# Kernel tuning notes

Hardware: AMD Instinct MI355X
Metric: run time of the kernel (lower is better)

Reference implementation:

```python
import jax, jax.numpy as jnp
import numpy as np

N_NODES = 50000
N_EDGES = 800000
FEAT_SIZE = 4096
EMB = 30          # embedding_size
HID = 80          # hidden_size
VOCAB = 10
HEADS = 2
TEMP = 1.0
GAT_SLOPE = 0.2   # DGL GATConv leaky_relu negative_slope
CONV_SLOPE = 0.01 # torch LeakyReLU default


def _lrelu(x, s):
    return jnp.where(x >= 0, x, s * x)


def gat_layer(feat, W, al, ar, b, src, dst, n_nodes):
    """DGL GATConv: feat [N, ..., Fin] -> [N, ..., H, Fout].
    W: [Fin, H*Fout]; al, ar, b: [H, Fout]."""
    H, F = al.shape
    z = jnp.tensordot(feat, W, axes=1).reshape(feat.shape[:-1] + (H, F))  # [N,...,H,F]
    el = (z * al).sum(-1, keepdims=True)  # [N,...,H,1]
    er = (z * ar).sum(-1, keepdims=True)
    e = _lrelu(el[src] + er[dst], GAT_SLOPE)            # [E,...,H,1]
    emax = jax.ops.segment_max(e, dst, num_segments=n_nodes)
    ex = jnp.exp(e - emax[dst])
    denom = jax.ops.segment_sum(ex, dst, num_segments=n_nodes)
    alpha = ex / denom[dst]                              # edge softmax per dst
    rst = jax.ops.segment_sum(z[src] * alpha, dst, num_segments=n_nodes)
    return rst + b


def setup_inputs() -> dict:
    key = jax.random.key(0)
    ks = jax.random.split(key, 24)
    s = 0.1
    return {
        "x": jax.random.normal(ks[0], (2, FEAT_SIZE), jnp.float32),
        "vocab": jax.random.normal(ks[1], (VOCAB,), jnp.float32),
        "node_feats": jax.random.normal(ks[2], (2, N_NODES, 3), jnp.float32),
        "src": jax.random.randint(ks[3], (2, N_EDGES), 0, N_NODES, jnp.int32),
        "dst": jax.random.randint(ks[4], (2, N_EDGES), 0, N_NODES, jnp.int32),
        "W_lin1": jax.random.normal(ks[5], (FEAT_SIZE, EMB), jnp.float32) * s,
        "Wc1": jax.random.normal(ks[6], (HID, 2), jnp.float32) * s,
        "Wc2": jax.random.normal(ks[7], (HID,), jnp.float32) * s,
        "gat1_W": jax.random.normal(ks[8], (3, HEADS * HID), jnp.float32) * s,
        "gat1_al": jax.random.normal(ks[9], (HEADS, HID), jnp.float32) * s,
        "gat1_ar": jax.random.normal(ks[10], (HEADS, HID), jnp.float32) * s,
        "gat1_b": jax.random.normal(ks[11], (HEADS, HID), jnp.float32) * s,
        "gat2_W": jax.random.normal(ks[12], (HID, HEADS * EMB), jnp.float32) * s,
        "gat2_al": jax.random.normal(ks[13], (HEADS, EMB), jnp.float32) * s,
        "gat2_ar": jax.random.normal(ks[14], (HEADS, EMB), jnp.float32) * s,
        "gat2_b": jax.random.normal(ks[15], (HEADS, EMB), jnp.float32) * s,
        "Wg1": jax.random.normal(ks[16], (2 * EMB, EMB), jnp.float32) * s,
        "bg1": jax.random.normal(ks[17], (EMB,), jnp.float32) * s,
        "W2": jax.random.normal(ks[18], (2 * EMB + VOCAB, HID), jnp.float32) * s,
        "W3": jax.random.normal(ks[19], (HID, 2), jnp.float32) * s,
    }


def reference(x, vocab, node_feats, src, dst, W_lin1, Wc1, Wc2,
              gat1_W, gat1_al, gat1_ar, gat1_b,
              gat2_W, gat2_al, gat2_ar, gat2_b,
              Wg1, bg1, W2, W3):
    # deterministic order = [0, 1] (original shuffles); order.index(0) == 0
    # image branch: per-game embedding -> [2, EMB]
    emb = x @ W_lin1                          # [2, EMB]
    h = _lrelu(Wc1 @ emb, CONV_SLOPE)         # im_conv1: [HID, EMB]
    h = _lrelu(Wc2 @ h, CONV_SLOPE)           # im_conv2: [EMB]
    # graph branch: two GAT layers per graph, mean over nodes, take head 0
    gr_emb = []
    for i in range(2):
        g1 = gat_layer(node_feats[i], gat1_W, gat1_al, gat1_ar, gat1_b,
                       src[i], dst[i], N_NODES)          # [N, H, HID]
        g1 = jax.nn.relu(g1)
        g2 = gat_layer(g1, gat2_W, gat2_al, gat2_ar, gat2_b,
                       src[i], dst[i], N_NODES)          # [N, H, H, EMB]
        a = g2.mean(axis=0)[0, 0]                        # mean_nodes then a[0][0][0] -> [EMB]
        gr_emb.append(a)
    gr = jnp.concatenate(gr_emb) @ Wg1 + bg1             # [EMB]
    hc = jnp.concatenate([gr, h, vocab])                 # [2*EMB + VOCAB]
    logits = jax.nn.log_softmax(((hc @ W2) @ W3) * (1.0 / TEMP), axis=0)
    return logits, 0
```

## Files before the change

kernel.cpp:

```cpp
#include <hip/hip_runtime.h>
#include <math.h>

#define NN 50000
#define NE 800000

#define CH 196
#define C  256
#define CAP 3600
#define BSL 8192

__device__ __forceinline__ float lrelu(float x, float s) { return x >= 0.f ? x : s * x; }

__global__ __launch_bounds__(1024) void k_pre(
        const float* __restrict__ x, const float* __restrict__ Wl,
        const float* __restrict__ nodef,
        const float* __restrict__ W1, const float* __restrict__ al1,
        const float* __restrict__ ar1,
        const int* __restrict__ src, const int* __restrict__ dst,
        float* __restrict__ imgp, float* __restrict__ feat4,
        float* __restrict__ er1, unsigned* __restrict__ gctr,
        unsigned* __restrict__ dbin, unsigned* __restrict__ sbin) {
    int bid = blockIdx.x, t = threadIdx.x;
    if (bid < 16) {
        __shared__ float part[32][64];
        int kk = t & 31, rq = t >> 5;
        int r0 = bid * 256;
        float a0 = 0.f, a1 = 0.f;
        if (kk < 30) {
            for (int i = 0; i < 8; ++i) {
                int r = r0 + rq * 8 + i;
                float wv = Wl[r * 30 + kk];
                a0 += x[r] * wv;
                a1 += x[4096 + r] * wv;
            }
        }
        part[rq][kk] = a0;
        part[rq][32 + kk] = a1;
        __syncthreads();
        if (t < 60) {
            int g = t / 30, k = t - g * 30;
            float s = 0.f;
            #pragma unroll
            for (int rr = 0; rr < 32; ++rr) s += part[rr][g * 32 + k];
            imgp[bid * 64 + g * 32 + k] = s;
        }
    } else if (bid < 114) {
        __shared__ float sP[6];
        if (t < 6) {
            int c = t >> 1;
            const float* av = (t & 1) ? ar1 : al1;
            float s = 0.f;
            for (int f = 0; f < 80; ++f) s += W1[c * 160 + f] * av[f];
            sP[(t & 1) * 3 + c] = s;
        }
        __syncthreads();
        int flat = (bid - 16) * 1024 + t;
        if (flat < 2 * NN) {
            int g = flat / NN;
            int n = flat - g * NN;
            const float* f = nodef + (size_t)flat * 3;
            float f0 = f[0], f1 = f[1], f2 = f[2];
            *(float4*)(feat4 + (size_t)flat * 4) =
                make_float4(f0, f1, f2, f0 * sP[0] + f1 * sP[1] + f2 * sP[2]);
            er1[g * NN + n] = f0 * sP[3] + f1 * sP[4] + f2 * sP[5];
        }
    } else {
        __shared__ unsigned scnt[C];
        __shared__ unsigned sstart[C + 1];
        __shared__ unsigned sbase[C];
        __shared__ unsigned sofs[C];
        __shared__ unsigned ssort[BSL];
        int b3 = bid - 114;
        int a = b3 / 196;
        int rem = b3 - a * 196;
        int g = rem / 98;
        int bx = rem - g * 98;
        if (t < C) scnt[t] = 0;
        __syncthreads();
        const int* ip = (a ? src : dst) + (size_t)g * NE;
        const int* pp = (a ? dst : src) + (size_t)g * NE;
        unsigned* bin = (a ? sbin : dbin);
        int cbase = (a * 2 + g) * C;
        int bbase = g * C;
        int e0 = bx * BSL + t * 8;
        int nv = 0;
        if (e0 < NE) nv = (NE - e0) < 8 ? (NE - e0) : 8;
        unsigned pk[8];
        if (nv == 8) {
            int4 v0 = *(const int4*)(ip + e0), v1 = *(const int4*)(ip + e0 + 4);
            int4 q0 = *(const int4*)(pp + e0), q1 = *(const int4*)(pp + e0 + 4);
            int dj[8] = {v0.x, v0.y, v0.z, v0.w, v1.x, v1.y, v1.z, v1.w};
            int pj[8] = {q0.x, q0.y, q0.z, q0.w, q1.x, q1.y, q1.z, q1.w};
            #pragma unroll
            for (int j = 0; j < 8; ++j) {
                unsigned c = (unsigned)dj[j] / CH;
                pk[j] = (c << 24) | (((unsigned)dj[j] - c * CH) << 16) | (unsigned)pj[j];
                atomicAdd(&scnt[c], 1u);
            }
        } else {
            for (int j = 0; j < nv; ++j) {
                int dv = ip[e0 + j], pv = pp[e0 + j];
                unsigned c = (unsigned)dv / CH;
                pk[j] = (c << 24) | (((unsigned)dv - c * CH) << 16) | (unsigned)pv;
                atomicAdd(&scnt[c], 1u);
            }
        }
        __syncthreads();
        if (t == 0) {
            unsigned run = 0;
            for (int j = 0; j < C; ++j) { sstart[j] = run; run += scnt[j]; }
            sstart[C] = run;
        }
        __syncthreads();
        if (t < C) {
            sbase[t] = atomicAdd(&gctr[cbase + t], scnt[t]);
            sofs[t] = sstart[t];
        }
        __syncthreads();
        for (int j = 0; j < nv; ++j) {
            unsigned c = pk[j] >> 24;
            unsigned slot = atomicAdd(&sofs[c], 1u);
            ssort[slot] = pk[j];
        }
        __syncthreads();
        unsigned total = sstart[C];
        for (unsigned i = t; i < total; i += 1024) {
            unsigned v = ssort[i];
            unsigned c = v >> 24;
            unsigned pos = sbase[c] + (i - sstart[c]);
            if (pos < CAP) bin[(size_t)(bbase + c) * CAP + pos] = v & 0xFFFFFFu;
        }
    }
}

__global__ __launch_bounds__(1024) void k_e1n(const unsigned* __restrict__ dbin,
                                              const unsigned* __restrict__ gctr,
                                              const float* __restrict__ feat4,
                                              const float* __restrict__ er1,
                                              const float* __restrict__ W1,
                                              const float* __restrict__ b1,
                                              const float* __restrict__ W2,
                                              const float* __restrict__ al2,
                                              const float* __restrict__ ar2,
                                              float* __restrict__ facc4,
                                              float* __restrict__ el2,
                                              float* __restrict__ er2iv) {
    __shared__ unsigned scnt[CH];
    __shared__ unsigned sstart[CH + 1];
    __shared__ unsigned sofs[CH];
    __shared__ unsigned ssort[CAP];
    __shared__ float sEr[CH];
    __shared__ float pacc[8][CH];
    __shared__ float sW[240], sB[80], sU[80], sV[80];
    int c = blockIdx.x, g = blockIdx.y, t = threadIdx.x;
    int base = c * CH;
    if (t < CH) {
        scnt[t] = 0;
        sEr[t] = (base + t < NN) ? er1[(size_t)g * NN + base + t] : 0.f;
    }
    if (t >= 1024 - 80) {
        int f = t - (1024 - 80);
        sW[f] = W1[f];
        sW[80 + f] = W1[160 + f];
        sW[160 + f] = W1[320 + f];
        sB[f] = b1[f];
        float u = 0.f, v = 0.f;
        for (int j = 0; j < 30; ++j) {
            float wv = W2[f * 60 + j];
            u += wv * al2[j];
            v += wv * ar2[j];
        }
        sU[f] = u;
        sV[f] = v;
    }
    __syncthreads();
    const unsigned* seg = dbin + (size_t)(g * C + c) * CAP;
    unsigned size = gctr[g * C + c];
    if (size > CAP) size = CAP;
    for (unsigned i = t; i < size; i += 1024) atomicAdd(&scnt[seg[i] >> 16], 1u);
    __syncthreads();
    if (t == 0) {
        unsigned run = 0;
        for (int j = 0; j < CH; ++j) { sstart[j] = run; run += scnt[j]; }
        sstart[CH] = run;
    }
    __syncthreads();
    if (t < CH) sofs[t] = sstart[t];
    __syncthreads();
    for (unsigned i = t; i < size; i += 1024) {
        unsigned p = seg[i];
        unsigned slot = atomicAdd(&sofs[p >> 16], 1u);
        ssort[slot] = p & 0xFFFFu;
    }
    __syncthreads();
    const float* f4 = feat4 + (size_t)g * NN * 4;
    if (t < 2 * CH) {
        int rel = t >> 1, half = t & 1;
        unsigned start = sstart[rel], end = sstart[rel + 1];
        unsigned mid = (start + end) >> 1;
        unsigned lo = half ? mid : start;
        unsigned hi = half ? end : mid;
        float ax = 0.f, ay = 0.f, az = 0.f, aw = 0.f;
        float erv = sEr[rel];
        for (unsigned j = lo; j < hi; ++j) {
            unsigned s = ssort[j];
            float4 F = *(const float4*)(f4 + (size_t)s * 4);
            float wv = __expf(lrelu(F.w + erv, 0.2f));
            ax += wv * F.x; ay += wv * F.y; az += wv * F.z; aw += wv;
        }
        int hb = half * 4;
        pacc[hb + 0][rel] = ax;
        pacc[hb + 1][rel] = ay;
        pacc[hb + 2][rel] = az;
        pacc[hb + 3][rel] = aw;
    }
    __syncthreads();
    if (t < CH && base + t < NN) {
        size_t n = (size_t)g * NN + base + t;
        float fx = pacc[0][t] + pacc[4][t];
        float fy = pacc[1][t] + pacc[5][t];
        float fz = pacc[2][t] + pacc[6][t];
        float fw = pacc[3][t] + pacc[7][t];
        *(float4*)(facc4 + n * 4) = make_float4(fx, fy, fz, fw);
        float inv = fw != 0.f ? 1.f / fw : 0.f;
        float c0 = fx * inv, c1 = fy * inv, c2 = fz * inv;
        float el = 0.f, er = 0.f;
        #pragma unroll
        for (int f = 0; f < 80; ++f) {
            float gg = c0 * sW[f] + c1 * sW[80 + f] + c2 * sW[160 + f] + sB[f];
            gg = gg > 0.f ? gg : 0.f;
            el += gg * sU[f];
            er += gg * sV[f];
        }
        el2[n] = el;
        er2iv[n * 2] = er;
    }
}

__global__ __launch_bounds__(1024) void k_e2d(const unsigned* __restrict__ dbin,
                                              const unsigned* __restrict__ gctr,
                                              const float* __restrict__ el2,
                                              float* __restrict__ er2iv) {
    __shared__ float sden[CH], sEr2[CH];
    int c = blockIdx.x, g = blockIdx.y, t = threadIdx.x;
    int base = c * CH;
    if (t < CH) {
        sden[t] = 0.f;
        sEr2[t] = (base + t < NN) ? er2iv[((size_t)g * NN + base + t) * 2] : 0.f;
    }
    __syncthreads();
    const float* el = el2 + (size_t)g * NN;
    const unsigned* seg = dbin + (size_t)(g * C + c) * CAP;
    unsigned size = gctr[g * C + c];
    if (size > CAP) size = CAP;
    for (unsigned i = t; i < size; i += 1024) {
        unsigned p = seg[i];
        unsigned rel = p >> 16;
        atomicAdd(&sden[rel], __expf(lrelu(el[p & 0xFFFFu] + sEr2[rel], 0.2f)));
    }
    __syncthreads();
    if (t < CH && base + t < NN) {
        float s = sden[t];
        er2iv[((size_t)g * NN + base + t) * 2 + 1] = s != 0.f ? 1.f / s : 0.f;
    }
}

__global__ __launch_bounds__(1024) void k_e3q(const unsigned* __restrict__ sbin,
                                              const unsigned* __restrict__ gctr,
                                              const float* __restrict__ el2,
                                              const float* __restrict__ er2iv,
                                              const float* __restrict__ facc4,
                                              const float* __restrict__ W1,
                                              const float* __restrict__ b1,
                                              float* __restrict__ Apart) {
    __shared__ float sq[CH], sEl[CH];
    __shared__ float cx[CH], cy[CH], cz[CH];
    __shared__ float pacc2[12][80];
    __shared__ float sW[240], sB[80];
    int c = blockIdx.x, g = blockIdx.y, t = threadIdx.x;
    int base = c * CH;
    if (t < CH) {
        sq[t] = 0.f;
        sEl[t] = (base + t < NN) ? el2[(size_t)g * NN + base + t] : 0.f;
    }
    if (t >= 1024 - 80) {
        int f = t - (1024 - 80);
        sW[f] = W1[f];
        sW[80 + f] = W1[160 + f];
        sW[160 + f] = W1[320 + f];
        sB[f] = b1[f];
    }
    __syncthreads();
    const float* er = er2iv + (size_t)g * NN * 2;
    const unsigned* seg = sbin + (size_t)(g * C + c) * CAP;
    unsigned size = gctr[(2 + g) * C + c];
    if (size > CAP) size = CAP;
    for (unsigned i = t; i < size; i += 1024) {
        unsigned p = seg[i];
        unsigned rel = p >> 16;
        float2 E = *(const float2*)(er + 2 * (size_t)(p & 0xFFFFu));
        atomicAdd(&sq[rel], __expf(lrelu(sEl[rel] + E.x, 0.2f)) * E.y);
    }
    __syncthreads();
    if (t < CH) {
        if (base + t < NN) {
            float4 fa = *(const float4*)(facc4 + ((size_t)g * NN + base + t) * 4);
            float inv = fa.w != 0.f ? 1.f / fa.w : 0.f;
            cx[t] = fa.x * inv; cy[t] = fa.y * inv; cz[t] = fa.z * inv;
        } else {
            cx[t] = 0.f; cy[t] = 0.f; cz[t] = 0.f;
        }
    }
    __syncthreads();
    int grp = t / 80, f = t - grp * 80;
    if (grp < 12) {
        float acc = 0.f;
        float wf0 = sW[f], wf1 = sW[80 + f], wf2 = sW[160 + f], bf = sB[f];
        for (int i = grp; i < CH; i += 12) {
            float qn = sq[i];
            float gg = cx[i] * wf0 + cy[i] * wf1 + cz[i] * wf2 + bf;
            gg = gg > 0.f ? gg : 0.f;
            acc += qn * gg;
        }
        pacc2[grp][f] = acc;
    }
    __syncthreads();
    if (t < 80) {
        float s = 0.f;
        #pragma unroll
        for (int j = 0; j < 12; ++j) s += pacc2[j][t];
        Apart[((size_t)g * C + c) * 80 + t] = s;
    }
}

__global__ void k_final(const float* __restrict__ Apart, const float* __restrict__ imgp,
                        const float* __restrict__ W2g, const float* __restrict__ b2,
                        const float* __restrict__ Wg1, const float* __restrict__ bg1,
                        const float* __restrict__ Wc1, const float* __restrict__ Wc2,
                        const float* __restrict__ vocab, const float* __restrict__ W2f,
                        const float* __restrict__ W3, float* __restrict__ out, int out_size) {
    __shared__ float sA[160];
    __shared__ float emb[60];
    __shared__ float hh[80 * 30];
    __shared__ float a[60];
    __shared__ float hc[70];
    __shared__ float tt[80];
    __shared__ float lp[2];
    int t = threadIdx.x;
    if (t < 160) {
        int g = t / 80, f = t - g * 80;
        float s = 0.f;
        const float* Ap = Apart + (size_t)g * C * 80 + f;
        for (int c = 0; c < C; ++c) s += Ap[(size_t)c * 80];
        sA[t] = s;
    } else if (t < 220) {
        int q = t - 160;
        int g = q / 30, j = q - g * 30;
        float s = 0.f;
        for (int b = 0; b < 16; ++b) s += imgp[b * 64 + g * 32 + j];
        emb[q] = s;
    }
    __syncthreads();
    if (t < 60) {
        int i = t / 30, j = t % 30;
        float acc = 0.f;
        for (int f = 0; f < 80; ++f) acc += sA[i * 80 + f] * W2g[f * 60 + j];
        a[t] = acc * (1.f / NN) + b2[j];
    }
    __syncthreads();
    for (int p = t; p < 2400; p += 256) {
        int i = p / 30, j = p % 30;
        float v = Wc1[i * 2 + 0] * emb[j] + Wc1[i * 2 + 1] * emb[30 + j];
        hh[p] = lrelu(v, 0.01f);
    }
    __syncthreads();
    if (t < 30) {
        float acc = 0.f;
        for (int i = 0; i < 80; ++i) acc += Wc2[i] * hh[i * 30 + t];
        hc[30 + t] = lrelu(acc, 0.01f);
        float acg = bg1[t];
        for (int j = 0; j < 60; ++j) acg += a[j] * Wg1[j * 30 + t];
        hc[t] = acg;
        if (t < 10) hc[60 + t] = vocab[t];
    }
    __syncthreads();
    if (t < 80) {
        float acc = 0.f;
        for (int qd = 0; qd < 70; ++qd) acc += hc[qd] * W2f[qd * 80 + t];
        tt[t] = acc;
    }
    __syncthreads();
    if (t < 2) {
        float acc = 0.f;
        for (int p = 0; p < 80; ++p) acc += tt[p] * W3[p * 2 + t];
        lp[t] = acc;
    }
    __syncthreads();
    if (t == 0) {
        float m = fmaxf(lp[0], lp[1]);
        float lse = m + logf(expf(lp[0] - m) + expf(lp[1] - m));
        out[0] = lp[0] - lse;
        out[1] = lp[1] - lse;
    }
    for (int i = 2 + t; i < out_size; i += blockDim.x) out[i] = 0.f;
}

extern "C" void kernel_launch(void* const* d_in, const int* in_sizes, int n_in,
                              void* d_out, int out_size, void* d_ws, size_t ws_size,
                              hipStream_t stream) {
    const float* x        = (const float*)d_in[0];
    const float* vocab    = (const float*)d_in[1];
    const float* nodef    = (const float*)d_in[2];
    const int*   src      = (const int*)d_in[3];
    const int*   dst      = (const int*)d_in[4];
    const float* W_lin1   = (const float*)d_in[5];
    const float* Wc1      = (const float*)d_in[6];
    const float* Wc2      = (const float*)d_in[7];
    const float* gat1_W   = (const float*)d_in[8];
    const float* gat1_al  = (const float*)d_in[9];
    const float* gat1_ar  = (const float*)d_in[10];
    const float* gat1_b   = (const float*)d_in[11];
    const float* gat2_W   = (const float*)d_in[12];
    const float* gat2_al  = (const float*)d_in[13];
    const float* gat2_ar  = (const float*)d_in[14];
    const float* gat2_b   = (const float*)d_in[15];
    const float* Wg1      = (const float*)d_in[16];
    const float* bg1      = (const float*)d_in[17];
    const float* W2       = (const float*)d_in[18];
    const float* W3       = (const float*)d_in[19];
    (void)in_sizes; (void)n_in; (void)ws_size;

    float* w = (float*)d_ws;
    size_t off = 0;
    auto alloc = [&](size_t n) { size_t o = off; off += (n + 63) & ~(size_t)63; return o; };
    size_t o_ctr  = alloc(1024);
    size_t o_imgp = alloc(16 * 64);
    size_t o_Ap   = alloc((size_t)2 * C * 80);
    size_t o_feat = alloc((size_t)2 * NN * 4);
    size_t o_er1  = alloc(2 * NN);
    size_t o_el2  = alloc(2 * NN);
    size_t o_eriv = alloc((size_t)2 * NN * 2);
    size_t o_facc = alloc((size_t)2 * NN * 4);
    size_t o_dbin = alloc((size_t)2 * C * CAP);
    size_t o_sbin = alloc((size_t)2 * C * CAP);
    unsigned* gctr = (unsigned*)(w + o_ctr);
    unsigned* dbin = (unsigned*)(w + o_dbin);
    unsigned* sbin = (unsigned*)(w + o_sbin);

    hipMemsetAsync(w + o_ctr, 0, 1024 * sizeof(float), stream);
    k_pre<<<506, 1024, 0, stream>>>(x, W_lin1, nodef, gat1_W, gat1_al, gat1_ar,
                                    src, dst, w + o_imgp, w + o_feat, w + o_er1,
                                    gctr, dbin, sbin);

    k_e1n<<<dim3(C, 2), 1024, 0, stream>>>(dbin, gctr, w + o_feat, w + o_er1,
                                           gat1_W, gat1_b, gat2_W, gat2_al, gat2_ar,
                                           w + o_facc, w + o_el2, w + o_eriv);

    k_e2d<<<dim3(C, 2), 1024, 0, stream>>>(dbin, gctr, w + o_el2, w + o_eriv);

    k_e3q<<<dim3(C, 2), 1024, 0, stream>>>(sbin, gctr, w + o_el2, w + o_eriv,
                                           w + o_facc, gat1_W, gat1_b, w + o_Ap);

    k_final<<<1, 256, 0, stream>>>(w + o_Ap, w + o_imgp, gat2_W, gat2_b, Wg1, bg1,
                                   Wc1, Wc2, vocab, W2, W3, (float*)d_out, out_size);
}
```

Measured before the change: 86.40 us.

## Merge dst/src binning blocks, split edge accumulation four ways, widen final reduction

The binning stage of k_pre now handles both the dst-keyed and src-keyed bins in one block, so each edge chunk's src and dst indices are read once instead of twice, and the grid shrinks from 506 to 310 blocks. Shared memory is unioned across the three block roles, and the doubled sort buffers raise per-block LDS use. k_e1n splits each node's edge range across four threads instead of two to shorten serial loops on high-degree nodes. k_final runs with 1024 threads and does its partial sums in parallel groups, cutting the serial reduction length in that single-block tail kernel.

Measured after the change: 86.68 us. About the same (+0.3%).

```diff
diff --git a/kernel.cpp b/kernel.cpp
--- a/kernel.cpp
+++ b/kernel.cpp
@@ -20,9 +20,19 @@
         float* __restrict__ imgp, float* __restrict__ feat4,
         float* __restrict__ er1, unsigned* __restrict__ gctr,
         unsigned* __restrict__ dbin, unsigned* __restrict__ sbin) {
+    __shared__ union {
+        struct { float part[32][64]; } img;
+        struct { float sP[6]; } pack;
+        struct {
+            unsigned scnt[2][C];
+            unsigned sstart[2][C + 1];
+            unsigned sbase[2][C];
+            unsigned sofs[2][C];
+            unsigned ssort[2][BSL];
+        } bin;
+    } sm;
     int bid = blockIdx.x, t = threadIdx.x;
     if (bid < 16) {
-        __shared__ float part[32][64];
         int kk = t & 31, rq = t >> 5;
         int r0 = bid * 256;
         float a0 = 0.f, a1 = 0.f;
@@ -34,24 +44,23 @@
                 a1 += x[4096 + r] * wv;
             }
         }
-        part[rq][kk] = a0;
-        part[rq][32 + kk] = a1;
+        sm.img.part[rq][kk] = a0;
+        sm.img.part[rq][32 + kk] = a1;
         __syncthreads();
         if (t < 60) {
             int g = t / 30, k = t - g * 30;
             float s = 0.f;
             #pragma unroll
-            for (int rr = 0; rr < 32; ++rr) s += part[rr][g * 32 + k];
+            for (int rr = 0; rr < 32; ++rr) s += sm.img.part[rr][g * 32 + k];
             imgp[bid * 64 + g * 32 + k] = s;
         }
     } else if (bid < 114) {
-        __shared__ float sP[6];
         if (t < 6) {
             int c = t >> 1;
             const float* av = (t & 1) ? ar1 : al1;
             float s = 0.f;
             for (int f = 0; f < 80; ++f) s += W1[c * 160 + f] * av[f];
-            sP[(t & 1) * 3 + c] = s;
+            sm.pack.sP[(t & 1) * 3 + c] = s;
         }
         __syncthreads();
         int flat = (bid - 16) * 1024 + t;
@@ -61,74 +70,83 @@
             const float* f = nodef + (size_t)flat * 3;
             float f0 = f[0], f1 = f[1], f2 = f[2];
             *(float4*)(feat4 + (size_t)flat * 4) =
-                make_float4(f0, f1, f2, f0 * sP[0] + f1 * sP[1] + f2 * sP[2]);
-            er1[g * NN + n] = f0 * sP[3] + f1 * sP[4] + f2 * sP[5];
+                make_float4(f0, f1, f2,
+                            f0 * sm.pack.sP[0] + f1 * sm.pack.sP[1] + f2 * sm.pack.sP[2]);
+            er1[g * NN + n] = f0 * sm.pack.sP[3] + f1 * sm.pack.sP[4] + f2 * sm.pack.sP[5];
         }
     } else {
-        __shared__ unsigned scnt[C];
-        __shared__ unsigned sstart[C + 1];
-        __shared__ unsigned sbase[C];
-        __shared__ unsigned sofs[C];
-        __shared__ unsigned ssort[BSL];
         int b3 = bid - 114;
-        int a = b3 / 196;
-        int rem = b3 - a * 196;
-        int g = rem / 98;
-        int bx = rem - g * 98;
-        if (t < C) scnt[t] = 0;
-        __syncthreads();
-        const int* ip = (a ? src : dst) + (size_t)g * NE;
-        const int* pp = (a ? dst : src) + (size_t)g * NE;
-        unsigned* bin = (a ? sbin : dbin);
-        int cbase = (a * 2 + g) * C;
-        int bbase = g * C;
+        int g = b3 / 98;
+        int bx = b3 - g * 98;
+        if (t < 2 * C) sm.bin.scnt[t >> 8][t & 255] = 0;
+        __syncthreads();
+        const int* dp = dst + (size_t)g * NE;
+        const int* sp = src + (size_t)g * NE;
         int e0 = bx * BSL + t * 8;
         int nv = 0;
         if (e0 < NE) nv = (NE - e0) < 8 ? (NE - e0) : 8;
-        unsigned pk[8];
+        unsigned pkd[8], pks[8];
         if (nv == 8) {
-            int4 v0 = *(const int4*)(ip + e0), v1 = *(const int4*)(ip + e0 + 4);
-            int4 q0 = *(const int4*)(pp + e0), q1 = *(const int4*)(pp + e0 + 4);
-            int dj[8] = {v0.x, v0.y, v0.z, v0.w, v1.x, v1.y, v1.z, v1.w};
-            int pj[8] = {q0.x, q0.y, q0.z, q0.w, q1.x, q1.y, q1.z, q1.w};
+            int4 d0 = *(const int4*)(dp + e0), d1 = *(const int4*)(dp + e0 + 4);
+            int4 s0 = *(const int4*)(sp + e0), s1 = *(const int4*)(sp + e0 + 4);
+            int dj[8] = {d0.x, d0.y, d0.z, d0.w, d1.x, d1.y, d1.z, d1.w};
+            int sj[8] = {s0.x, s0.y, s0.z, s0.w, s1.x, s1.y, s1.z, s1.w};
             #pragma unroll
             for (int j = 0; j < 8; ++j) {
-                unsigned c = (unsigned)dj[j] / CH;
-                pk[j] = (c << 24) | (((unsigned)dj[j] - c * CH) << 16) | (unsigned)pj[j];
-                atomicAdd(&scnt[c], 1u);
+                unsigned cd = (unsigned)dj[j] / CH;
+                pkd[j] = (cd << 24) | (((unsigned)dj[j] - cd * CH) << 16) | (unsigned)sj[j];
+                atomicAdd(&sm.bin.scnt[0][cd], 1u);
+                unsigned cs = (unsigned)sj[j] / CH;
+                pks[j] = (cs << 24) | (((unsigned)sj[j] - cs * CH) << 16) | (unsigned)dj[j];
+                atomicAdd(&sm.bin.scnt[1][cs], 1u);
             }
         } else {
             for (int j = 0; j < nv; ++j) {
-                int dv = ip[e0 + j], pv = pp[e0 + j];
-                unsigned c = (unsigned)dv / CH;
-                pk[j] = (c << 24) | (((unsigned)dv - c * CH) << 16) | (unsigned)pv;
-                atomicAdd(&scnt[c], 1u);
+                int dv = dp[e0 + j], sv = sp[e0 + j];
+                unsigned cd = (unsigned)dv / CH;
+                pkd[j] = (cd << 24) | (((unsigned)dv - cd * CH) << 16) | (unsigned)sv;
+                atomicAdd(&sm.bin.scnt[0][cd], 1u);
+                unsigned cs = (unsigned)sv / CH;
+                pks[j] = (cs << 24) | (((unsigned)sv - cs * CH) << 16) | (unsigned)dv;
+                atomicAdd(&sm.bin.scnt[1][cs], 1u);
             }
         }
         __syncthreads();
-        if (t == 0) {
+        if (t < 2) {
             unsigned run = 0;
-            for (int j = 0; j < C; ++j) { sstart[j] = run; run += scnt[j]; }
-            sstart[C] = run;
-        }
-        __syncthreads();
-        if (t < C) {
-            sbase[t] = atomicAdd(&gctr[cbase + t], scnt[t]);
-            sofs[t] = sstart[t];
+            for (int j = 0; j < C; ++j) { sm.bin.sstart[t][j] = run; run += sm.bin.scnt[t][j]; }
+            sm.bin.sstart[t][C] = run;
+        }
+        __syncthreads();
+        if (t < 2 * C) {
+            int a = t >> 8, c = t & 255;
+            sm.bin.sbase[a][c] = atomicAdd(&gctr[(a * 2 + g) * C + c], sm.bin.scnt[a][c]);
+            sm.bin.sofs[a][c] = sm.bin.sstart[a][c];
         }
         __syncthreads();
         for (int j = 0; j < nv; ++j) {
-            unsigned c = pk[j] >> 24;
-            unsigned slot = atomicAdd(&sofs[c], 1u);
-            ssort[slot] = pk[j];
-        }
-        __syncthreads();
-        unsigned total = sstart[C];
-        for (unsigned i = t; i < total; i += 1024) {
-            unsigned v = ssort[i];
+            unsigned c = pkd[j] >> 24;
+            unsigned slot = atomicAdd(&sm.bin.sofs[0][c], 1u);
+            sm.bin.ssort[0][slot] = pkd[j];
+            c = pks[j] >> 24;
+            slot = atomicAdd(&sm.bin.sofs[1][c], 1u);
+            sm.bin.ssort[1][slot] = pks[j];
+        }
+        __syncthreads();
+        int bbase = g * C;
+        unsigned tot0 = sm.bin.sstart[0][C];
+        for (unsigned i = t; i < tot0; i += 1024) {
+            unsigned v = sm.bin.ssort[0][i];
             unsigned c = v >> 24;
-            unsigned pos = sbase[c] + (i - sstart[c]);
-            if (pos < CAP) bin[(size_t)(bbase + c) * CAP + pos] = v & 0xFFFFFFu;
+            unsigned pos = sm.bin.sbase[0][c] + (i - sm.bin.sstart[0][c]);
+            if (pos < CAP) dbin[(size_t)(bbase + c) * CAP + pos] = v & 0xFFFFFFu;
+        }
+        unsigned tot1 = sm.bin.sstart[1][C];
+        for (unsigned i = t; i < tot1; i += 1024) {
+            unsigned v = sm.bin.ssort[1][i];
+            unsigned c = v >> 24;
+            unsigned pos = sm.bin.sbase[1][c] + (i - sm.bin.sstart[1][c]);
+            if (pos < CAP) sbin[(size_t)(bbase + c) * CAP + pos] = v & 0xFFFFFFu;
         }
     }
 }
@@ -150,7 +168,7 @@
     __shared__ unsigned sofs[CH];
     __shared__ unsigned ssort[CAP];
     __shared__ float sEr[CH];
-    __shared__ float pacc[8][CH];
+    __shared__ float pacc[16][CH];
     __shared__ float sW[240], sB[80], sU[80], sV[80];
     int c = blockIdx.x, g = blockIdx.y, t = threadIdx.x;
     int base = c * CH;
@@ -194,12 +212,12 @@
     }
     __syncthreads();
     const float* f4 = feat4 + (size_t)g * NN * 4;
-    if (t < 2 * CH) {
-        int rel = t >> 1, half = t & 1;
+    if (t < 4 * CH) {
+        int rel = t >> 2, quar = t & 3;
         unsigned start = sstart[rel], end = sstart[rel + 1];
-        unsigned mid = (start + end) >> 1;
-        unsigned lo = half ? mid : start;
-        unsigned hi = half ? end : mid;
+        unsigned len = end - start;
+        unsigned lo = start + (len * quar) / 4;
+        unsigned hi = start + (len * (quar + 1)) / 4;
         float ax = 0.f, ay = 0.f, az = 0.f, aw = 0.f;
         float erv = sEr[rel];
         for (unsigned j = lo; j < hi; ++j) {
@@ -208,19 +226,19 @@
             float wv = __expf(lrelu(F.w + erv, 0.2f));
             ax += wv * F.x; ay += wv * F.y; az += wv * F.z; aw += wv;
         }
-        int hb = half * 4;
-        pacc[hb + 0][rel] = ax;
-        pacc[hb + 1][rel] = ay;
-        pacc[hb + 2][rel] = az;
-        pacc[hb + 3][rel] = aw;
+        int qb = quar * 4;
+        pacc[qb + 0][rel] = ax;
+        pacc[qb + 1][rel] = ay;
+        pacc[qb + 2][rel] = az;
+        pacc[qb + 3][rel] = aw;
     }
     __syncthreads();
     if (t < CH && base + t < NN) {
         size_t n = (size_t)g * NN + base + t;
-        float fx = pacc[0][t] + pacc[4][t];
-        float fy = pacc[1][t] + pacc[5][t];
-        float fz = pacc[2][t] + pacc[6][t];
-        float fw = pacc[3][t] + pacc[7][t];
+        float fx = pacc[0][t] + pacc[4][t] + pacc[8][t] + pacc[12][t];
+        float fy = pacc[1][t] + pacc[5][t] + pacc[9][t] + pacc[13][t];
+        float fz = pacc[2][t] + pacc[6][t] + pacc[10][t] + pacc[14][t];
+        float fw = pacc[3][t] + pacc[7][t] + pacc[11][t] + pacc[15][t];
         *(float4*)(facc4 + n * 4) = make_float4(fx, fy, fz, fw);
         float inv = fw != 0.f ? 1.f / fw : 0.f;
         float c0 = fx * inv, c1 = fy * inv, c2 = fz * inv;
@@ -333,12 +351,15 @@
     }
 }
 
-__global__ void k_final(const float* __restrict__ Apart, const float* __restrict__ imgp,
-                        const float* __restrict__ W2g, const float* __restrict__ b2,
-                        const float* __restrict__ Wg1, const float* __restrict__ bg1,
-                        const float* __restrict__ Wc1, const float* __restrict__ Wc2,
-                        const float* __restrict__ vocab, const float* __restrict__ W2f,
-                        const float* __restrict__ W3, float* __restrict__ out, int out_size) {
+__global__ __launch_bounds__(1024) void k_final(
+        const float* __restrict__ Apart, const float* __restrict__ imgp,
+        const float* __restrict__ W2g, const float* __restrict__ b2,
+        const float* __restrict__ Wg1, const float* __restrict__ bg1,
+        const float* __restrict__ Wc1, const float* __restrict__ Wc2,
+        const float* __restrict__ vocab, const float* __restrict__ W2f,
+        const float* __restrict__ W3, float* __restrict__ out, int out_size) {
+    __shared__ float pA[160 * 4];
+    __shared__ float pE[60 * 4];
     __shared__ float sA[160];
     __shared__ float emb[60];
     __shared__ float hh[80 * 30];
@@ -347,18 +368,26 @@
     __shared__ float tt[80];
     __shared__ float lp[2];
     int t = threadIdx.x;
-    if (t < 160) {
-        int g = t / 80, f = t - g * 80;
+    if (t < 640) {
+        int g = t / 320, r = t - g * 320;
+        int grp = r / 80, f = r - grp * 80;
         float s = 0.f;
-        const float* Ap = Apart + (size_t)g * C * 80 + f;
-        for (int c = 0; c < C; ++c) s += Ap[(size_t)c * 80];
-        sA[t] = s;
-    } else if (t < 220) {
+        const float* Ap = Apart + ((size_t)g * C + grp * 64) * 80 + f;
+        for (int c = 0; c < 64; ++c) s += Ap[(size_t)c * 80];
+        pA[(g * 80 + f) * 4 + grp] = s;
+    } else if (t < 880) {
+        int q = t - 640;
+        int gj = q >> 2, grp = q & 3;
+        int g = gj / 30, j = gj - g * 30;
+        float s = 0.f;
+        for (int b = grp; b < 16; b += 4) s += imgp[b * 64 + g * 32 + j];
+        pE[gj * 4 + grp] = s;
+    }
+    __syncthreads();
+    if (t < 160) sA[t] = pA[t * 4] + pA[t * 4 + 1] + pA[t * 4 + 2] + pA[t * 4 + 3];
+    else if (t < 220) {
         int q = t - 160;
-        int g = q / 30, j = q - g * 30;
-        float s = 0.f;
-        for (int b = 0; b < 16; ++b) s += imgp[b * 64 + g * 32 + j];
-        emb[q] = s;
+        emb[q] = pE[q * 4] + pE[q * 4 + 1] + pE[q * 4 + 2] + pE[q * 4 + 3];
     }
     __syncthreads();
     if (t < 60) {
@@ -368,7 +397,7 @@
         a[t] = acc * (1.f / NN) + b2[j];
     }
     __syncthreads();
-    for (int p = t; p < 2400; p += 256) {
+    for (int p = t; p < 2400; p += 1024) {
         int i = p / 30, j = p % 30;
         float v = Wc1[i * 2 + 0] * emb[j] + Wc1[i * 2 + 1] * emb[30 + j];
         hh[p] = lrelu(v, 0.01f);
@@ -448,7 +477,7 @@
     unsigned* sbin = (unsigned*)(w + o_sbin);
 
     hipMemsetAsync(w + o_ctr, 0, 1024 * sizeof(float), stream);
-    k_pre<<<506, 1024, 0, stream>>>(x, W_lin1, nodef, gat1_W, gat1_al, gat1_ar,
+    k_pre<<<310, 1024, 0, stream>>>(x, W_lin1, nodef, gat1_W, gat1_al, gat1_ar,
                                     src, dst, w + o_imgp, w + o_feat, w + o_er1,
                                     gctr, dbin, sbin);
 
@@ -461,6 +490,6 @@
     k_e3q<<<dim3(C, 2), 1024, 0, stream>>>(sbin, gctr, w + o_el2, w + o_eriv,
                                            w + o_facc, gat1_W, gat1_b, w + o_Ap);
 
-    k_final<<<1, 256, 0, stream>>>(w + o_Ap, w + o_imgp, gat2_W, gat2_b, Wg1, bg1,
-                                   Wc1, Wc2, vocab, W2, W3, (float*)d_out, out_size);
-}
+    k_final<<<1, 1024, 0, stream>>>(w + o_Ap, w + o_imgp, gat2_W, gat2_b, Wg1, bg1,
+                                    Wc1, Wc2, vocab, W2, W3, (float*)d_out, out_size);
+}
```
